# Kernel optimization log

Hardware: AMD Instinct MI355X
Metric: run time of the kernel (lower is better)

## Reference

```python
import jax, jax.numpy as jnp
import numpy as np
from functools import partial

NPOINT, NSAMPLE = 1024, 32
EPS = 1e-5

def setup_inputs() -> dict:
    key = jax.random.key(0)
    ks = jax.random.split(key, 16)
    B, N, C = 16, 4096, 64
    d = {
        "xyz": jax.random.normal(ks[0], (B, N, 3), jnp.float32),
        "points": jax.random.normal(ks[1], (B, N, C), jnp.float32),
    }
    chans = [67, 64, 64, 128]
    for i in range(3):
        cin, cout = chans[i], chans[i + 1]
        d[f"w{i+1}"] = jax.random.normal(ks[2 + i], (cout, cin), jnp.float32) * (1.0 / np.sqrt(cin))
        d[f"b{i+1}"] = jnp.zeros((cout,), jnp.float32)
        d[f"g{i+1}"] = jnp.ones((cout,), jnp.float32)
        d[f"be{i+1}"] = jnp.zeros((cout,), jnp.float32)
    return d

def farthest_point_sample(xyz, npoint):
    # xyz: (B, N, 3); deterministic start index 0 (torch code uses randint)
    B, N, _ = xyz.shape
    bidx = jnp.arange(B)

    def step(carry, _):
        distance, farthest = carry
        centroid = xyz[bidx, farthest]                       # (B, 3)
        dist = jnp.sum((xyz - centroid[:, None, :]) ** 2, -1)  # (B, N)
        distance = jnp.minimum(distance, dist)
        return (distance, jnp.argmax(distance, axis=1)), farthest

    init = (jnp.full((B, N), 1e10, xyz.dtype), jnp.zeros((B,), jnp.int32))
    _, centroids = jax.lax.scan(step, init, None, length=npoint)  # (npoint, B)
    return centroids.T                                            # (B, npoint)

def knn_group(nsample, xyz, new_xyz, points):
    # xyz: (B,N,3), new_xyz: (B,S,3), points: (B,N,C)
    # squared distances (same topk ordering as cdist)
    d2 = (jnp.sum(new_xyz ** 2, -1)[:, :, None]
          + jnp.sum(xyz ** 2, -1)[:, None, :]
          - 2.0 * jnp.einsum("bsd,bnd->bsn", new_xyz, xyz))     # (B,S,N)
    _, idx = jax.lax.top_k(-d2, nsample)                          # (B,S,K)

    gather = jax.vmap(lambda feats, i: feats[i])                  # per-batch fancy index
    grouped_xyz = gather(xyz, idx) - new_xyz[:, :, None, :]       # (B,S,K,3)
    grouped_pts = jnp.concatenate([grouped_xyz, gather(points, idx)], -1)  # (B,S,K,3+C)
    return grouped_xyz, grouped_pts

def mlp_layer(x, w, b, g, be):
    # 1x1 conv + BatchNorm (batch stats, training mode) + ReLU
    y = jnp.einsum("bskc,oc->bsko", x, w) + b
    mu = jnp.mean(y, axis=(0, 1, 2))
    var = jnp.var(y, axis=(0, 1, 2))
    y = (y - mu) * jax.lax.rsqrt(var + EPS) * g + be
    return jax.nn.relu(y)

def reference(xyz, points, w1, b1, g1, be1, w2, b2, g2, be2, w3, b3, g3, be3):
    centroids = farthest_point_sample(xyz, NPOINT)                    # (B,S)
    new_xyz = jnp.take_along_axis(xyz, centroids[:, :, None], axis=1)  # (B,S,3)
    _, x = knn_group(NSAMPLE, xyz, new_xyz, points)                   # (B,S,K,3+C)
    x = mlp_layer(x, w1, b1, g1, be1)
    x = mlp_layer(x, w2, b2, g2, be2)
    x = mlp_layer(x, w3, b3, g3, be3)
    new_points = jnp.max(x, axis=2)                                   # (B,S,mlp[-1])
    return new_xyz, new_points
```

## Files before the change

kernel.cpp:

```cpp
#include <hip/hip_runtime.h>

typedef unsigned int   uint;
typedef unsigned short ushort;
typedef unsigned long long u64;
typedef float f32x4 __attribute__((ext_vector_type(4)));

__device__ __forceinline__ void dot16x2(const float* __restrict__ wr,
                                        const f32x4* xa, const f32x4* xb,
                                        float& accA, float& accB){
#pragma unroll
  for (int k=0;k<4;k++){
    f32x4 w=*(const f32x4*)(wr+4*k);
    accA=fmaf(xa[k][0],w[0],accA); accA=fmaf(xa[k][1],w[1],accA);
    accA=fmaf(xa[k][2],w[2],accA); accA=fmaf(xa[k][3],w[3],accA);
    accB=fmaf(xb[k][0],w[0],accB); accB=fmaf(xb[k][1],w[1],accB);
    accB=fmaf(xb[k][2],w[2],accB); accB=fmaf(xb[k][3],w[3],accB);
  }
}

__global__ __launch_bounds__(256) void k_fps(const float* __restrict__ xyz,
                                             int* __restrict__ cent,
                                             float* __restrict__ oxyz){
  __shared__ __align__(16) float sp[4096][4];
  __shared__ u64 rk[2][4];
  __shared__ int sel[1024];
  const int b = blockIdx.x, tid = threadIdx.x, lane=tid&63, wave=tid>>6;
  const float* xb = xyz + (long)b*4096*3;
  float px[16], py[16], pz[16], pd[16];
#pragma unroll
  for (int j=0;j<16;j++){
    int n = tid + 256*j;
    float x=xb[n*3], y=xb[n*3+1], z=xb[n*3+2];
    sp[n][0]=x; sp[n][1]=y; sp[n][2]=z; sp[n][3]=0.0f;
    px[j]=x; py[j]=y; pz[j]=z; pd[j]=1e10f;
  }
  if (tid==0) sel[0]=0;
  __syncthreads();
  int f = 0;
  for (int t=1;t<1024;t++){
    f32x4 c = *(const f32x4*)sp[f];
    float bv=-1.0f; int bi=0;
#pragma unroll
    for (int j=0;j<16;j++){
      int n = tid + 256*j;
      float dx=px[j]-c[0], dy=py[j]-c[1], dz=pz[j]-c[2];
      float d=__fadd_rn(__fadd_rn(__fmul_rn(dx,dx),__fmul_rn(dy,dy)),__fmul_rn(dz,dz));
      float mn=fminf(pd[j],d); pd[j]=mn;
      if (j==0){ bv=mn; bi=n; }
      else if (mn>bv){ bv=mn; bi=n; }
    }
    u64 key = ((u64)__float_as_uint(bv)<<32) | (uint)(~bi);
#pragma unroll
    for (int off=32;off;off>>=1){
      u64 ok=__shfl_xor(key,off);
      key = ok>key ? ok : key;
    }
    int par=t&1;
    if (lane==0) rk[par][wave]=key;
    __syncthreads();
    {
      u64 k0=rk[par][0], k1=rk[par][1], k2=rk[par][2], k3=rk[par][3];
      u64 ka = k0>k1?k0:k1;
      u64 kb = k2>k3?k2:k3;
      u64 kk = ka>kb?ka:kb;
      f = (int)(~(uint)kk) & 4095;
    }
    if (tid==0) sel[t]=f;
  }
  __syncthreads();
#pragma unroll
  for (int j=0;j<4;j++){
    int s = tid + 256*j;
    int n = sel[s];
    cent[b*1024+s]=n;
    f32x4 cf=*(const f32x4*)sp[n];
    oxyz[(b*1024+s)*3+0]=cf[0];
    oxyz[(b*1024+s)*3+1]=cf[1];
    oxyz[(b*1024+s)*3+2]=cf[2];
  }
}

__global__ __launch_bounds__(256) void k_knn(const float* __restrict__ xyz,
                                             const int* __restrict__ cent,
                                             ushort* __restrict__ kidx){
  __shared__ float sx[4096], sy[4096], sz[4096];
  const int bx=blockIdx.x, b=bx>>5, chunk=bx&31;
  const int tid=threadIdx.x, lane=tid&63, wave=tid>>6;
  const float* xb = xyz + (long)b*4096*3;
#pragma unroll
  for (int j=0;j<16;j++){
    int n = tid + 256*j;
    sx[n]=xb[n*3]; sy[n]=xb[n*3+1]; sz[n]=xb[n*3+2];
  }
  __syncthreads();
  const u64 SENT=~0ull;
  for (int qi=0; qi<8; qi++){
    int s = chunk*32 + wave*8 + qi;
    int qn = cent[b*1024 + s] & 4095;
    double qx=(double)sx[qn], qy=(double)sy[qn], qz=(double)sz[qn];
    u64 k1=SENT, k2=SENT;
#pragma unroll 8
    for (int j=0;j<64;j++){
      int n = lane + 64*j;
      double dx=(double)sx[n]-qx, dy=(double)sy[n]-qy, dz=(double)sz[n]-qz;
      double d2 = dx*dx + dy*dy + dz*dz;
      u64 kd = (((u64)__double_as_longlong(d2)) & ~4095ull) | (uint)n;
      if (kd<k1){ k2=k1; k1=kd; }
      else if (kd<k2){ k2=kd; }
    }
    u64 removed=0ull;
    ushort* outp = kidx + (b*1024 + s)*32;
    for (int r=0;r<32;r++){
      u64 wk=k1;
#pragma unroll
      for (int off=32;off;off>>=1){
        u64 ok=__shfl_xor(wk,off);
        wk = ok<wk ? ok : wk;
      }
      if (lane==0) outp[r]=(ushort)(wk & 4095u);
      if (wk==k1){
        removed |= 1ull << (((uint)(k1&4095u))>>6);
        if (k2!=SENT){ k1=k2; k2=SENT; }
        else {
          k1=SENT; k2=SENT;
#pragma unroll 8
          for (int j=0;j<64;j++){
            if ((removed>>j)&1ull) continue;
            int n = lane + 64*j;
            double dx=(double)sx[n]-qx, dy=(double)sy[n]-qy, dz=(double)sz[n]-qz;
            double d2 = dx*dx + dy*dy + dz*dz;
            u64 kd = (((u64)__double_as_longlong(d2)) & ~4095ull) | (uint)n;
            if (kd<k1){ k2=k1; k1=kd; }
            else if (kd<k2){ k2=kd; }
          }
        }
      }
    }
  }
}


__global__ __launch_bounds__(256) void k_mlp1b(const float* __restrict__ xyz,
                                               const float* __restrict__ pts,
                                               const float* __restrict__ w1,
                                               const float* __restrict__ b1,
                                               const int* __restrict__ cent,
                                               const ushort* __restrict__ kidx,
                                               float* __restrict__ part,
                                               float* __restrict__ y){
  __shared__ __align__(16) float L[9760];
  float* W1  = L;
  float* XIN = L+4384;
  float* WRED= L+8736;
  const int tid=threadIdx.x, bi=blockIdx.x;
  const int row=tid>>3, oc=tid&7, wave=tid>>6;
  const int b=bi>>6, s0=(bi&63)*16;
  const long bN=(long)b*4096;

  for (int i=tid;i<64*68;i+=256){
    int r=i/68, c=i-r*68;
    float v = (c<64)? w1[r*67+3+c] : (c<67? w1[r*67+(c-64)] : 0.0f);
    W1[r*68+((r>>3)<<2)+c]=v;
  }
  float breg1[8];
#pragma unroll
  for (int i=0;i<8;i++) breg1[i]=b1[oc*8+i];
  float ps[8], pq[8];
#pragma unroll
  for (int s=0;s<8;s++){ ps[s]=0.f; pq[s]=0.f; }
  __syncthreads();

  for (int t=0; t<8; t++){
    int sgA = b*1024 + s0 + t*2, sgB = sgA+1;
    {
      int nA = kidx[sgA*32+row] & 4095;
      int nB = kidx[sgB*32+row] & 4095;
      const float* prA = pts + (bN+nA)*64;
      const float* prB = pts + (bN+nB)*64;
      *(f32x4*)(XIN + row*68 + oc*8)          = *(const f32x4*)(prA + oc*8);
      *(f32x4*)(XIN + row*68 + oc*8 + 4)      = *(const f32x4*)(prA + oc*8 + 4);
      *(f32x4*)(XIN + (row+32)*68 + oc*8)     = *(const f32x4*)(prB + oc*8);
      *(f32x4*)(XIN + (row+32)*68 + oc*8 + 4) = *(const f32x4*)(prB + oc*8 + 4);
      if (oc==0){
        int qA = cent[sgA] & 4095, qB = cent[sgB] & 4095;
        const float* xpA = xyz + (bN+nA)*3; const float* qpA = xyz + (bN+qA)*3;
        const float* xpB = xyz + (bN+nB)*3; const float* qpB = xyz + (bN+qB)*3;
        XIN[row*68+64]=xpA[0]-qpA[0]; XIN[row*68+65]=xpA[1]-qpA[1];
        XIN[row*68+66]=xpA[2]-qpA[2]; XIN[row*68+67]=0.0f;
        XIN[(row+32)*68+64]=xpB[0]-qpB[0]; XIN[(row+32)*68+65]=xpB[1]-qpB[1];
        XIN[(row+32)*68+66]=xpB[2]-qpB[2]; XIN[(row+32)*68+67]=0.0f;
      }
    }
    const float* xrowA = XIN + row*68;
    const float* xrowB = XIN + (row+32)*68;
    float acc[2][8];
#pragma unroll
    for (int i=0;i<8;i++){ acc[0][i]=breg1[i]; acc[1][i]=breg1[i]; }
#pragma unroll
    for (int co=0;co<4;co++){
      f32x4 xa[4], xbv[4];
#pragma unroll
      for (int k=0;k<4;k++){ xa[k]=*(const f32x4*)(xrowA+co*16+4*k); xbv[k]=*(const f32x4*)(xrowB+co*16+4*k); }
#pragma unroll
      for (int i=0;i<8;i++)
        dot16x2(W1+(oc*8+i)*68+(oc<<2)+co*16, xa, xbv, acc[0][i], acc[1][i]);
    }
    {
      f32x4 xtA=*(const f32x4*)(xrowA+64), xtB=*(const f32x4*)(xrowB+64);
#pragma unroll
      for (int i=0;i<8;i++){
        const float* wr=W1+(oc*8+i)*68+(oc<<2)+64;
        f32x4 w=*(const f32x4*)wr;
        acc[0][i]=fmaf(xtA[0],w[0],acc[0][i]); acc[0][i]=fmaf(xtA[1],w[1],acc[0][i]);
        acc[0][i]=fmaf(xtA[2],w[2],acc[0][i]); acc[0][i]=fmaf(xtA[3],w[3],acc[0][i]);
        acc[1][i]=fmaf(xtB[0],w[0],acc[1][i]); acc[1][i]=fmaf(xtB[1],w[1],acc[1][i]);
        acc[1][i]=fmaf(xtB[2],w[2],acc[1][i]); acc[1][i]=fmaf(xtB[3],w[3],acc[1][i]);
      }
    }
    {
      long baseA = ((long)sgA*32+row)*64 + oc*8;
      long baseB = ((long)sgB*32+row)*64 + oc*8;
      *(f32x4*)(y+baseA)   = (f32x4){acc[0][0],acc[0][1],acc[0][2],acc[0][3]};
      *(f32x4*)(y+baseA+4) = (f32x4){acc[0][4],acc[0][5],acc[0][6],acc[0][7]};
      *(f32x4*)(y+baseB)   = (f32x4){acc[1][0],acc[1][1],acc[1][2],acc[1][3]};
      *(f32x4*)(y+baseB+4) = (f32x4){acc[1][4],acc[1][5],acc[1][6],acc[1][7]};
    }
#pragma unroll
    for (int i=0;i<8;i++){
      ps[i]+=acc[0][i]+acc[1][i];
      pq[i]=fmaf(acc[0][i],acc[0][i],pq[i]); pq[i]=fmaf(acc[1][i],acc[1][i],pq[i]);
    }
  }
#pragma unroll
  for (int s=0;s<8;s++){
    ps[s]+=__shfl_xor(ps[s],8); ps[s]+=__shfl_xor(ps[s],16); ps[s]+=__shfl_xor(ps[s],32);
    pq[s]+=__shfl_xor(pq[s],8); pq[s]+=__shfl_xor(pq[s],16); pq[s]+=__shfl_xor(pq[s],32);
  }
  __syncthreads();
  if ((tid&63)<8){
    for (int s=0;s<8;s++){
      WRED[((wave*8+oc)*16+s)*2+0]=ps[s];
      WRED[((wave*8+oc)*16+s)*2+1]=pq[s];
    }
  }
  __syncthreads();
  if (tid<64){
    int o=tid, occ=o>>3, i=o&7;
    float s=0.f,q=0.f;
#pragma unroll
    for (int w=0;w<4;w++){ s+=WRED[((w*8+occ)*16+i)*2]; q+=WRED[((w*8+occ)*16+i)*2+1]; }
    part[(bi*64+o)*2]=s; part[(bi*64+o)*2+1]=q;
  }
}

__global__ __launch_bounds__(256) void k_mlp2b(const float* __restrict__ w2,
                                               const float* __restrict__ b2,
                                               const float* __restrict__ ab1,
                                               float* __restrict__ part,
                                               float* __restrict__ y){
  __shared__ __align__(16) float L[9504];
  float* W2  = L;
  float* XIN = L+4128;
  float* WRED= L+8480;
  const int tid=threadIdx.x, bi=blockIdx.x;
  const int row=tid>>3, oc=tid&7, wave=tid>>6;
  const int b=bi>>6, s0=(bi&63)*16;

  for (int i=tid;i<4096;i+=256){
    int r=i>>6, c=i&63;
    W2[r*64+((r>>3)<<2)+c]=w2[i];
  }
  float areg1[8],creg1[8],breg2[8];
#pragma unroll
  for (int i=0;i<8;i++){ int ch=oc*8+i; areg1[i]=ab1[ch*2]; creg1[i]=ab1[ch*2+1]; breg2[i]=b2[ch]; }
  float ps[8], pq[8];
#pragma unroll
  for (int s=0;s<8;s++){ ps[s]=0.f; pq[s]=0.f; }
  __syncthreads();

  for (int t=0; t<8; t++){
    int sgA = b*1024 + s0 + t*2, sgB = sgA+1;
    long baseA = ((long)sgA*32+row)*64 + oc*8;
    long baseB = ((long)sgB*32+row)*64 + oc*8;
    {
      f32x4 ya0=*(const f32x4*)(y+baseA), ya1=*(const f32x4*)(y+baseA+4);
      f32x4 yb0=*(const f32x4*)(y+baseB), yb1=*(const f32x4*)(y+baseB+4);
      f32x4 xo;
      xo[0]=fmaxf(fmaf(areg1[0],ya0[0],creg1[0]),0.0f);
      xo[1]=fmaxf(fmaf(areg1[1],ya0[1],creg1[1]),0.0f);
      xo[2]=fmaxf(fmaf(areg1[2],ya0[2],creg1[2]),0.0f);
      xo[3]=fmaxf(fmaf(areg1[3],ya0[3],creg1[3]),0.0f);
      *(f32x4*)(XIN+row*68+oc*8)=xo;
      xo[0]=fmaxf(fmaf(areg1[4],ya1[0],creg1[4]),0.0f);
      xo[1]=fmaxf(fmaf(areg1[5],ya1[1],creg1[5]),0.0f);
      xo[2]=fmaxf(fmaf(areg1[6],ya1[2],creg1[6]),0.0f);
      xo[3]=fmaxf(fmaf(areg1[7],ya1[3],creg1[7]),0.0f);
      *(f32x4*)(XIN+row*68+oc*8+4)=xo;
      xo[0]=fmaxf(fmaf(areg1[0],yb0[0],creg1[0]),0.0f);
      xo[1]=fmaxf(fmaf(areg1[1],yb0[1],creg1[1]),0.0f);
      xo[2]=fmaxf(fmaf(areg1[2],yb0[2],creg1[2]),0.0f);
      xo[3]=fmaxf(fmaf(areg1[3],yb0[3],creg1[3]),0.0f);
      *(f32x4*)(XIN+(row+32)*68+oc*8)=xo;
      xo[0]=fmaxf(fmaf(areg1[4],yb1[0],creg1[4]),0.0f);
      xo[1]=fmaxf(fmaf(areg1[5],yb1[1],creg1[5]),0.0f);
      xo[2]=fmaxf(fmaf(areg1[6],yb1[2],creg1[6]),0.0f);
      xo[3]=fmaxf(fmaf(areg1[7],yb1[3],creg1[7]),0.0f);
      *(f32x4*)(XIN+(row+32)*68+oc*8+4)=xo;
    }
    const float* x2A = XIN + row*68;
    const float* x2B = XIN + (row+32)*68;
    float acc2[2][8];
#pragma unroll
    for (int i=0;i<8;i++){ acc2[0][i]=breg2[i]; acc2[1][i]=breg2[i]; }
#pragma unroll
    for (int co=0;co<4;co++){
      f32x4 xa[4], xbv[4];
#pragma unroll
      for (int k=0;k<4;k++){ xa[k]=*(const f32x4*)(x2A+co*16+4*k); xbv[k]=*(const f32x4*)(x2B+co*16+4*k); }
#pragma unroll
      for (int i=0;i<8;i++)
        dot16x2(W2+(oc*8+i)*64+(oc<<2)+co*16, xa, xbv, acc2[0][i], acc2[1][i]);
    }
    *(f32x4*)(y+baseA)   = (f32x4){acc2[0][0],acc2[0][1],acc2[0][2],acc2[0][3]};
    *(f32x4*)(y+baseA+4) = (f32x4){acc2[0][4],acc2[0][5],acc2[0][6],acc2[0][7]};
    *(f32x4*)(y+baseB)   = (f32x4){acc2[1][0],acc2[1][1],acc2[1][2],acc2[1][3]};
    *(f32x4*)(y+baseB+4) = (f32x4){acc2[1][4],acc2[1][5],acc2[1][6],acc2[1][7]};
#pragma unroll
    for (int i=0;i<8;i++){
      ps[i]+=acc2[0][i]+acc2[1][i];
      pq[i]=fmaf(acc2[0][i],acc2[0][i],pq[i]); pq[i]=fmaf(acc2[1][i],acc2[1][i],pq[i]);
    }
  }
#pragma unroll
  for (int s=0;s<8;s++){
    ps[s]+=__shfl_xor(ps[s],8); ps[s]+=__shfl_xor(ps[s],16); ps[s]+=__shfl_xor(ps[s],32);
    pq[s]+=__shfl_xor(pq[s],8); pq[s]+=__shfl_xor(pq[s],16); pq[s]+=__shfl_xor(pq[s],32);
  }
  __syncthreads();
  if ((tid&63)<8){
    for (int s=0;s<8;s++){
      WRED[((wave*8+oc)*16+s)*2+0]=ps[s];
      WRED[((wave*8+oc)*16+s)*2+1]=pq[s];
    }
  }
  __syncthreads();
  if (tid<64){
    int o=tid, occ=o>>3, i=o&7;
    float s=0.f,q=0.f;
#pragma unroll
    for (int w=0;w<4;w++){ s+=WRED[((w*8+occ)*16+i)*2]; q+=WRED[((w*8+occ)*16+i)*2+1]; }
    part[(bi*64+o)*2]=s; part[(bi*64+o)*2+1]=q;
  }
}

__global__ __launch_bounds__(256) void k_mlp3b(const float* __restrict__ w3,
                                               const float* __restrict__ b3,
                                               const float* __restrict__ ab2,
                                               float* __restrict__ part,
                                               const float* __restrict__ y,
                                               float* __restrict__ mx){
  __shared__ __align__(16) float L[13696];
  float* W3F = L;
  float* XIN = L+8320;
  float* WRED= L+12672;
  const int tid=threadIdx.x, bi=blockIdx.x;
  const int row=tid>>3, oc=tid&7, wave=tid>>6;
  const int b=bi>>6, s0=(bi&63)*16;

  for (int i=tid;i<8192;i+=256){
    int og=i>>11, rem=i&2047, r=rem>>6, c=rem&63;
    W3F[og*2080 + r*64+((r>>2)<<2)+c]=w3[i];
  }
  float areg2[8],creg2[8];
#pragma unroll
  for (int i=0;i<8;i++){ int ch=oc*8+i; areg2[i]=ab2[ch*2]; creg2[i]=ab2[ch*2+1]; }
  float breg3[16];
#pragma unroll
  for (int og=0;og<4;og++)
#pragma unroll
    for (int i=0;i<4;i++) breg3[og*4+i]=b3[og*32+oc*4+i];
  float ps[16], pq[16];
#pragma unroll
  for (int s=0;s<16;s++){ ps[s]=0.f; pq[s]=0.f; }
  __syncthreads();

  for (int t=0; t<8; t++){
    int sgA = b*1024 + s0 + t*2, sgB = sgA+1;
    long baseA = ((long)sgA*32+row)*64 + oc*8;
    long baseB = ((long)sgB*32+row)*64 + oc*8;
    {
      f32x4 ya0=*(const f32x4*)(y+baseA), ya1=*(const f32x4*)(y+baseA+4);
      f32x4 yb0=*(const f32x4*)(y+baseB), yb1=*(const f32x4*)(y+baseB+4);
      f32x4 xo;
      xo[0]=fmaxf(fmaf(areg2[0],ya0[0],creg2[0]),0.0f);
      xo[1]=fmaxf(fmaf(areg2[1],ya0[1],creg2[1]),0.0f);
      xo[2]=fmaxf(fmaf(areg2[2],ya0[2],creg2[2]),0.0f);
      xo[3]=fmaxf(fmaf(areg2[3],ya0[3],creg2[3]),0.0f);
      *(f32x4*)(XIN+row*68+oc*8)=xo;
      xo[0]=fmaxf(fmaf(areg2[4],ya1[0],creg2[4]),0.0f);
      xo[1]=fmaxf(fmaf(areg2[5],ya1[1],creg2[5]),0.0f);
      xo[2]=fmaxf(fmaf(areg2[6],ya1[2],creg2[6]),0.0f);
      xo[3]=fmaxf(fmaf(areg2[7],ya1[3],creg2[7]),0.0f);
      *(f32x4*)(XIN+row*68+oc*8+4)=xo;
      xo[0]=fmaxf(fmaf(areg2[0],yb0[0],creg2[0]),0.0f);
      xo[1]=fmaxf(fmaf(areg2[1],yb0[1],creg2[1]),0.0f);
      xo[2]=fmaxf(fmaf(areg2[2],yb0[2],creg2[2]),0.0f);
      xo[3]=fmaxf(fmaf(areg2[3],yb0[3],creg2[3]),0.0f);
      *(f32x4*)(XIN+(row+32)*68+oc*8)=xo;
      xo[0]=fmaxf(fmaf(areg2[4],yb1[0],creg2[4]),0.0f);
      xo[1]=fmaxf(fmaf(areg2[5],yb1[1],creg2[5]),0.0f);
      xo[2]=fmaxf(fmaf(areg2[6],yb1[2],creg2[6]),0.0f);
      xo[3]=fmaxf(fmaf(areg2[7],yb1[3],creg2[7]),0.0f);
      *(f32x4*)(XIN+(row+32)*68+oc*8+4)=xo;
    }
    const float* x2A = XIN + row*68;
    const float* x2B = XIN + (row+32)*68;
    float acc3[4][2][4];
#pragma unroll
    for (int og=0;og<4;og++)
#pragma unroll
      for (int i=0;i<4;i++){ acc3[og][0][i]=breg3[og*4+i]; acc3[og][1][i]=breg3[og*4+i]; }
#pragma unroll
    for (int co=0;co<4;co++){
      f32x4 xa[4], xbv[4];
#pragma unroll
      for (int k=0;k<4;k++){ xa[k]=*(const f32x4*)(x2A+co*16+4*k); xbv[k]=*(const f32x4*)(x2B+co*16+4*k); }
#pragma unroll
      for (int og=0;og<4;og++)
#pragma unroll
        for (int i=0;i<4;i++)
          dot16x2(W3F+og*2080+(oc*4+i)*64+(oc<<2)+co*16, xa, xbv, acc3[og][0][i], acc3[og][1][i]);
    }
    float vm[2][16];
#pragma unroll
    for (int og=0;og<4;og++)
#pragma unroll
      for (int i=0;i<4;i++){
        int s=og*4+i;
        ps[s]+=acc3[og][0][i]+acc3[og][1][i];
        pq[s]=fmaf(acc3[og][0][i],acc3[og][0][i],pq[s]); pq[s]=fmaf(acc3[og][1][i],acc3[og][1][i],pq[s]);
        vm[0][s]=acc3[og][0][i]; vm[1][s]=acc3[og][1][i];
      }
    {
#pragma unroll
      for (int q=0;q<2;q++)
#pragma unroll
        for (int s=0;s<16;s++){
          vm[q][s]=fmaxf(vm[q][s],__shfl_xor(vm[q][s],8));
          vm[q][s]=fmaxf(vm[q][s],__shfl_xor(vm[q][s],16));
          vm[q][s]=fmaxf(vm[q][s],__shfl_xor(vm[q][s],32));
        }
      __syncthreads();
      if ((tid&63)<8){
#pragma unroll
        for (int q=0;q<2;q++)
#pragma unroll
          for (int s=0;s<16;s++) WRED[(q*32 + wave*8+oc)*16 + s]=vm[q][s];
      }
      __syncthreads();
      {
        int q=tid>>7, o=tid&127;
        int og=o>>5, occ=(o&31)>>2, s=og*4+(o&3);
        float v=WRED[(q*32 + 0*8+occ)*16+s];
        v=fmaxf(v,WRED[(q*32 + 1*8+occ)*16+s]);
        v=fmaxf(v,WRED[(q*32 + 2*8+occ)*16+s]);
        v=fmaxf(v,WRED[(q*32 + 3*8+occ)*16+s]);
        mx[(long)(q? sgB : sgA)*128+o]=v;
      }
    }
  }
  {
#pragma unroll
    for (int s=0;s<16;s++){
      ps[s]+=__shfl_xor(ps[s],8); ps[s]+=__shfl_xor(ps[s],16); ps[s]+=__shfl_xor(ps[s],32);
      pq[s]+=__shfl_xor(pq[s],8); pq[s]+=__shfl_xor(pq[s],16); pq[s]+=__shfl_xor(pq[s],32);
    }
    __syncthreads();
    if ((tid&63)<8){
      for (int s=0;s<16;s++){
        WRED[((wave*8+oc)*16+s)*2+0]=ps[s];
        WRED[((wave*8+oc)*16+s)*2+1]=pq[s];
      }
    }
    __syncthreads();
    if (tid<128){
      int o=tid, og=o>>5, occ=(o&31)>>2, i=o&3, s2=og*4+i;
      float s=0.f,q=0.f;
#pragma unroll
      for (int w=0;w<4;w++){ s+=WRED[((w*8+occ)*16+s2)*2]; q+=WRED[((w*8+occ)*16+s2)*2+1]; }
      part[(bi*128+o)*2]=s; part[(bi*128+o)*2+1]=q;
    }
  }
}

__global__ void k_red(const float* __restrict__ part,
                      const float* __restrict__ gam,
                      const float* __restrict__ bet,
                      float* __restrict__ ab, int nch, int nblk){
  __shared__ float red[4][128][2];
  const int tid=threadIdx.x, ch=tid%nch, seg=tid/nch;
  float s=0.f,q=0.f;
  for (int i=seg;i<nblk;i+=4){ s+=part[(i*nch+ch)*2]; q+=part[(i*nch+ch)*2+1]; }
  red[seg][ch][0]=s; red[seg][ch][1]=q;
  __syncthreads();
  if (seg==0){
    s=red[0][ch][0]+red[1][ch][0]+red[2][ch][0]+red[3][ch][0];
    q=red[0][ch][1]+red[1][ch][1]+red[2][ch][1]+red[3][ch][1];
    float mu=s*(1.0f/524288.0f);
    float var=q*(1.0f/524288.0f)-mu*mu;
    var=fmaxf(var,0.0f);
    float a=gam[ch]/sqrtf(var+1e-5f);
    float c=bet[ch]-mu*a;
    ab[ch*2]=a; ab[ch*2+1]=c;
  }
}

__global__ __launch_bounds__(256) void k_out(const float* __restrict__ mx,
                                             const float* __restrict__ ab3,
                                             float* __restrict__ onp){
  int i = (blockIdx.x*256 + threadIdx.x)*4;
  int ch = i & 127;
  f32x4 v = *(const f32x4*)(mx+i);
  f32x4 r;
  r[0]=fmaxf(fmaf(ab3[(ch+0)*2], v[0], ab3[(ch+0)*2+1]), 0.0f);
  r[1]=fmaxf(fmaf(ab3[(ch+1)*2], v[1], ab3[(ch+1)*2+1]), 0.0f);
  r[2]=fmaxf(fmaf(ab3[(ch+2)*2], v[2], ab3[(ch+2)*2+1]), 0.0f);
  r[3]=fmaxf(fmaf(ab3[(ch+3)*2], v[3], ab3[(ch+3)*2+1]), 0.0f);
  *(f32x4*)(onp+i)=r;
}

extern "C" void kernel_launch(void* const* d_in, const int* in_sizes, int n_in,
                              void* d_out, int out_size, void* d_ws, size_t ws_size,
                              hipStream_t stream){
  const float* xyz=(const float*)d_in[0];
  const float* pts=(const float*)d_in[1];
  const float* w1 =(const float*)d_in[2];
  const float* b1 =(const float*)d_in[3];
  const float* g1 =(const float*)d_in[4];
  const float* be1=(const float*)d_in[5];
  const float* w2 =(const float*)d_in[6];
  const float* b2 =(const float*)d_in[7];
  const float* g2 =(const float*)d_in[8];
  const float* be2=(const float*)d_in[9];
  const float* w3 =(const float*)d_in[10];
  const float* b3 =(const float*)d_in[11];
  const float* g3 =(const float*)d_in[12];
  const float* be3=(const float*)d_in[13];
  char* ws=(char*)d_ws;
  int*    cent=(int*)(ws);
  ushort* kidx=(ushort*)(ws+  65536);
  float*  p   =(float*)(ws+ 1114112);
  float*  ab1 =(float*)(ws+ 2162688);
  float*  ab2 =(float*)(ws+ 2163200);
  float*  ab3 =(float*)(ws+ 2163712);
  float*  mx  =(float*)(ws+ 2164736);
  float*  y   =(float*)(ws+16777216);
  float* oxyz=(float*)d_out;
  float* onp =oxyz + 16*1024*3;

  const bool bigws = ws_size >= 150994944ull;

  k_fps<<<16, 256, 0, stream>>>(xyz, cent, oxyz);
  k_knn<<<512, 256, 0, stream>>>(xyz, cent, kidx);
  if (bigws){
    k_mlp1b<<<1024, 256, 0, stream>>>(xyz, pts, w1, b1, cent, kidx, p, y);
    k_red<<<1, 256, 0, stream>>>(p, g1, be1, ab1, 64, 1024);
    k_mlp2b<<<1024, 256, 0, stream>>>(w2, b2, ab1, p, y);
    k_red<<<1, 256, 0, stream>>>(p, g2, be2, ab2, 64, 1024);
    k_mlp3b<<<1024, 256, 0, stream>>>(w3, b3, ab2, p, y, mx);
    k_red<<<1, 512, 0, stream>>>(p, g3, be3, ab3, 128, 1024);
  } else {
    k_mlp1b<<<1024, 256, 0, stream>>>(xyz, pts, w1, b1, cent, kidx, p, y);
    k_red<<<1, 256, 0, stream>>>(p, g1, be1, ab1, 64, 1024);
    k_mlp2b<<<1024, 256, 0, stream>>>(w2, b2, ab1, p, y);
    k_red<<<1, 256, 0, stream>>>(p, g2, be2, ab2, 64, 1024);
    k_mlp3b<<<1024, 256, 0, stream>>>(w3, b3, ab2, p, y, mx);
    k_red<<<1, 512, 0, stream>>>(p, g3, be3, ab3, 128, 1024);
  }
  k_out<<<2048, 256, 0, stream>>>(mx, ab3, onp);
}
```

Baseline: 2.031 ms.

## Fuse FPS and KNN into one persistent kernel with per-batch ready flags

Merges the farthest-point-sampling and KNN kernels into a single launch: the first 16 blocks run FPS per batch and publish a release flag, while the remaining blocks loop over KNN work units and spin-wait on the flag for their batch. This aims to remove the kernel boundary and let KNN work overlap with FPS tails. It adds a memset for the flags and relies on FPS blocks being resident before waiting blocks, which risks deadlock or waiting blocks occupying CUs during FPS.

After: 2.548 ms. 1.25x slower.

```diff
diff --git a/kernel.cpp b/kernel.cpp
--- a/kernel.cpp
+++ b/kernel.cpp
@@ -18,127 +18,140 @@
   }
 }
 
-__global__ __launch_bounds__(256) void k_fps(const float* __restrict__ xyz,
-                                             int* __restrict__ cent,
-                                             float* __restrict__ oxyz){
-  __shared__ __align__(16) float sp[4096][4];
-  __shared__ u64 rk[2][4];
-  __shared__ int sel[1024];
-  const int b = blockIdx.x, tid = threadIdx.x, lane=tid&63, wave=tid>>6;
-  const float* xb = xyz + (long)b*4096*3;
-  float px[16], py[16], pz[16], pd[16];
-#pragma unroll
-  for (int j=0;j<16;j++){
-    int n = tid + 256*j;
-    float x=xb[n*3], y=xb[n*3+1], z=xb[n*3+2];
-    sp[n][0]=x; sp[n][1]=y; sp[n][2]=z; sp[n][3]=0.0f;
-    px[j]=x; py[j]=y; pz[j]=z; pd[j]=1e10f;
-  }
-  if (tid==0) sel[0]=0;
-  __syncthreads();
-  int f = 0;
-  for (int t=1;t<1024;t++){
-    f32x4 c = *(const f32x4*)sp[f];
-    float bv=-1.0f; int bi=0;
+__global__ __launch_bounds__(256,2) void k_fk(const float* __restrict__ xyz,
+                                              int* __restrict__ cent,
+                                              float* __restrict__ oxyz,
+                                              ushort* __restrict__ kidx,
+                                              int* __restrict__ flags){
+  __shared__ __align__(16) char LU[69760];
+  const int bid=blockIdx.x, tid=threadIdx.x, lane=tid&63, wave=tid>>6;
+
+  if (bid < 16){
+    float (*sp)[4] = (float(*)[4])LU;
+    u64* rk  = (u64*)(LU + 65536);
+    int* sel = (int*)(LU + 65600);
+    const int b = bid;
+    const float* xb = xyz + (long)b*4096*3;
+    float px[16], py[16], pz[16], pd[16];
 #pragma unroll
     for (int j=0;j<16;j++){
       int n = tid + 256*j;
-      float dx=px[j]-c[0], dy=py[j]-c[1], dz=pz[j]-c[2];
-      float d=__fadd_rn(__fadd_rn(__fmul_rn(dx,dx),__fmul_rn(dy,dy)),__fmul_rn(dz,dz));
-      float mn=fminf(pd[j],d); pd[j]=mn;
-      if (j==0){ bv=mn; bi=n; }
-      else if (mn>bv){ bv=mn; bi=n; }
-    }
-    u64 key = ((u64)__float_as_uint(bv)<<32) | (uint)(~bi);
-#pragma unroll
-    for (int off=32;off;off>>=1){
-      u64 ok=__shfl_xor(key,off);
-      key = ok>key ? ok : key;
-    }
-    int par=t&1;
-    if (lane==0) rk[par][wave]=key;
+      float x=xb[n*3], y=xb[n*3+1], z=xb[n*3+2];
+      sp[n][0]=x; sp[n][1]=y; sp[n][2]=z; sp[n][3]=0.0f;
+      px[j]=x; py[j]=y; pz[j]=z; pd[j]=1e10f;
+    }
+    if (tid==0) sel[0]=0;
     __syncthreads();
-    {
-      u64 k0=rk[par][0], k1=rk[par][1], k2=rk[par][2], k3=rk[par][3];
-      u64 ka = k0>k1?k0:k1;
-      u64 kb = k2>k3?k2:k3;
-      u64 kk = ka>kb?ka:kb;
-      f = (int)(~(uint)kk) & 4095;
-    }
-    if (tid==0) sel[t]=f;
-  }
-  __syncthreads();
-#pragma unroll
-  for (int j=0;j<4;j++){
-    int s = tid + 256*j;
-    int n = sel[s];
-    cent[b*1024+s]=n;
-    f32x4 cf=*(const f32x4*)sp[n];
-    oxyz[(b*1024+s)*3+0]=cf[0];
-    oxyz[(b*1024+s)*3+1]=cf[1];
-    oxyz[(b*1024+s)*3+2]=cf[2];
-  }
-}
-
-__global__ __launch_bounds__(256) void k_knn(const float* __restrict__ xyz,
-                                             const int* __restrict__ cent,
-                                             ushort* __restrict__ kidx){
-  __shared__ float sx[4096], sy[4096], sz[4096];
-  const int bx=blockIdx.x, b=bx>>5, chunk=bx&31;
-  const int tid=threadIdx.x, lane=tid&63, wave=tid>>6;
-  const float* xb = xyz + (long)b*4096*3;
-#pragma unroll
-  for (int j=0;j<16;j++){
-    int n = tid + 256*j;
-    sx[n]=xb[n*3]; sy[n]=xb[n*3+1]; sz[n]=xb[n*3+2];
-  }
-  __syncthreads();
-  const u64 SENT=~0ull;
-  for (int qi=0; qi<8; qi++){
-    int s = chunk*32 + wave*8 + qi;
-    int qn = cent[b*1024 + s] & 4095;
-    double qx=(double)sx[qn], qy=(double)sy[qn], qz=(double)sz[qn];
-    u64 k1=SENT, k2=SENT;
+    int f = 0;
+    for (int t=1;t<1024;t++){
+      f32x4 c = *(const f32x4*)sp[f];
+      float bv=-1.0f; int bi=0;
+#pragma unroll
+      for (int j=0;j<16;j++){
+        int n = tid + 256*j;
+        float dx=px[j]-c[0], dy=py[j]-c[1], dz=pz[j]-c[2];
+        float d=__fadd_rn(__fadd_rn(__fmul_rn(dx,dx),__fmul_rn(dy,dy)),__fmul_rn(dz,dz));
+        float mn=fminf(pd[j],d); pd[j]=mn;
+        if (j==0){ bv=mn; bi=n; }
+        else if (mn>bv){ bv=mn; bi=n; }
+      }
+      u64 key = ((u64)__float_as_uint(bv)<<32) | (uint)(~bi);
+#pragma unroll
+      for (int off=32;off;off>>=1){
+        u64 ok=__shfl_xor(key,off);
+        key = ok>key ? ok : key;
+      }
+      int par=t&1;
+      if (lane==0) rk[par*4+wave]=key;
+      __syncthreads();
+      {
+        u64 k0=rk[par*4+0], k1=rk[par*4+1], k2=rk[par*4+2], k3=rk[par*4+3];
+        u64 ka = k0>k1?k0:k1;
+        u64 kb = k2>k3?k2:k3;
+        u64 kk = ka>kb?ka:kb;
+        f = (int)(~(uint)kk) & 4095;
+      }
+      if (tid==0) sel[t]=f;
+    }
+    __syncthreads();
+#pragma unroll
+    for (int j=0;j<4;j++){
+      int s = tid + 256*j;
+      int n = sel[s];
+      cent[b*1024+s]=n;
+      f32x4 cf=*(const f32x4*)sp[n];
+      oxyz[(b*1024+s)*3+0]=cf[0];
+      oxyz[(b*1024+s)*3+1]=cf[1];
+      oxyz[(b*1024+s)*3+2]=cf[2];
+    }
+    __threadfence();
+    __syncthreads();
+    if (tid==0)
+      __hip_atomic_store(&flags[b], 1, __ATOMIC_RELEASE, __HIP_MEMORY_SCOPE_AGENT);
+  } else {
+    float* sx=(float*)LU; float* sy=sx+4096; float* sz=sy+4096;
+    for (int u = bid-16; u < 512; u += 496){
+      const int b = u>>5, chunk = u&31;
+      if (tid==0){
+        while (__hip_atomic_load(&flags[b], __ATOMIC_ACQUIRE, __HIP_MEMORY_SCOPE_AGENT)==0)
+          __builtin_amdgcn_s_sleep(64);
+      }
+      __syncthreads();
+      const float* xb = xyz + (long)b*4096*3;
+#pragma unroll
+      for (int j=0;j<16;j++){
+        int n = tid + 256*j;
+        sx[n]=xb[n*3]; sy[n]=xb[n*3+1]; sz[n]=xb[n*3+2];
+      }
+      __syncthreads();
+      const u64 SENT=~0ull;
+      for (int qi=0; qi<8; qi++){
+        int s = chunk*32 + wave*8 + qi;
+        int qn = cent[b*1024 + s] & 4095;
+        double qx=(double)sx[qn], qy=(double)sy[qn], qz=(double)sz[qn];
+        u64 k1=SENT, k2=SENT;
 #pragma unroll 8
-    for (int j=0;j<64;j++){
-      int n = lane + 64*j;
-      double dx=(double)sx[n]-qx, dy=(double)sy[n]-qy, dz=(double)sz[n]-qz;
-      double d2 = dx*dx + dy*dy + dz*dz;
-      u64 kd = (((u64)__double_as_longlong(d2)) & ~4095ull) | (uint)n;
-      if (kd<k1){ k2=k1; k1=kd; }
-      else if (kd<k2){ k2=kd; }
-    }
-    u64 removed=0ull;
-    ushort* outp = kidx + (b*1024 + s)*32;
-    for (int r=0;r<32;r++){
-      u64 wk=k1;
-#pragma unroll
-      for (int off=32;off;off>>=1){
-        u64 ok=__shfl_xor(wk,off);
-        wk = ok<wk ? ok : wk;
-      }
-      if (lane==0) outp[r]=(ushort)(wk & 4095u);
-      if (wk==k1){
-        removed |= 1ull << (((uint)(k1&4095u))>>6);
-        if (k2!=SENT){ k1=k2; k2=SENT; }
-        else {
-          k1=SENT; k2=SENT;
+        for (int j=0;j<64;j++){
+          int n = lane + 64*j;
+          double dx=(double)sx[n]-qx, dy=(double)sy[n]-qy, dz=(double)sz[n]-qz;
+          double d2 = dx*dx + dy*dy + dz*dz;
+          u64 kd = (((u64)__double_as_longlong(d2)) & ~4095ull) | (uint)n;
+          if (kd<k1){ k2=k1; k1=kd; }
+          else if (kd<k2){ k2=kd; }
+        }
+        u64 removed=0ull;
+        ushort* outp = kidx + (b*1024 + s)*32;
+        for (int r=0;r<32;r++){
+          u64 wk=k1;
+#pragma unroll
+          for (int off=32;off;off>>=1){
+            u64 ok=__shfl_xor(wk,off);
+            wk = ok<wk ? ok : wk;
+          }
+          if (lane==0) outp[r]=(ushort)(wk & 4095u);
+          if (wk==k1){
+            removed |= 1ull << (((uint)(k1&4095u))>>6);
+            if (k2!=SENT){ k1=k2; k2=SENT; }
+            else {
+              k1=SENT; k2=SENT;
 #pragma unroll 8
-          for (int j=0;j<64;j++){
-            if ((removed>>j)&1ull) continue;
-            int n = lane + 64*j;
-            double dx=(double)sx[n]-qx, dy=(double)sy[n]-qy, dz=(double)sz[n]-qz;
-            double d2 = dx*dx + dy*dy + dz*dz;
-            u64 kd = (((u64)__double_as_longlong(d2)) & ~4095ull) | (uint)n;
-            if (kd<k1){ k2=k1; k1=kd; }
-            else if (kd<k2){ k2=kd; }
+              for (int j=0;j<64;j++){
+                if ((removed>>j)&1ull) continue;
+                int n = lane + 64*j;
+                double dx=(double)sx[n]-qx, dy=(double)sy[n]-qy, dz=(double)sz[n]-qz;
+                double d2 = dx*dx + dy*dy + dz*dz;
+                u64 kd = (((u64)__double_as_longlong(d2)) & ~4095ull) | (uint)n;
+                if (kd<k1){ k2=k1; k1=kd; }
+                else if (kd<k2){ k2=kd; }
+              }
+            }
           }
         }
       }
-    }
-  }
-}
-
+      __syncthreads();
+    }
+  }
+}
 
 __global__ __launch_bounds__(256) void k_mlp1b(const float* __restrict__ xyz,
                                                const float* __restrict__ pts,
@@ -554,28 +567,18 @@
   float*  ab2 =(float*)(ws+ 2163200);
   float*  ab3 =(float*)(ws+ 2163712);
   float*  mx  =(float*)(ws+ 2164736);
+  int*    flags=(int*)(ws+15728640);
   float*  y   =(float*)(ws+16777216);
   float* oxyz=(float*)d_out;
   float* onp =oxyz + 16*1024*3;
 
-  const bool bigws = ws_size >= 150994944ull;
-
-  k_fps<<<16, 256, 0, stream>>>(xyz, cent, oxyz);
-  k_knn<<<512, 256, 0, stream>>>(xyz, cent, kidx);
-  if (bigws){
-    k_mlp1b<<<1024, 256, 0, stream>>>(xyz, pts, w1, b1, cent, kidx, p, y);
-    k_red<<<1, 256, 0, stream>>>(p, g1, be1, ab1, 64, 1024);
-    k_mlp2b<<<1024, 256, 0, stream>>>(w2, b2, ab1, p, y);
-    k_red<<<1, 256, 0, stream>>>(p, g2, be2, ab2, 64, 1024);
-    k_mlp3b<<<1024, 256, 0, stream>>>(w3, b3, ab2, p, y, mx);
-    k_red<<<1, 512, 0, stream>>>(p, g3, be3, ab3, 128, 1024);
-  } else {
-    k_mlp1b<<<1024, 256, 0, stream>>>(xyz, pts, w1, b1, cent, kidx, p, y);
-    k_red<<<1, 256, 0, stream>>>(p, g1, be1, ab1, 64, 1024);
-    k_mlp2b<<<1024, 256, 0, stream>>>(w2, b2, ab1, p, y);
-    k_red<<<1, 256, 0, stream>>>(p, g2, be2, ab2, 64, 1024);
-    k_mlp3b<<<1024, 256, 0, stream>>>(w3, b3, ab2, p, y, mx);
-    k_red<<<1, 512, 0, stream>>>(p, g3, be3, ab3, 128, 1024);
-  }
+  hipMemsetAsync(flags, 0, 64, stream);
+  k_fk<<<512, 256, 0, stream>>>(xyz, cent, oxyz, kidx, flags);
+  k_mlp1b<<<1024, 256, 0, stream>>>(xyz, pts, w1, b1, cent, kidx, p, y);
+  k_red<<<1, 256, 0, stream>>>(p, g1, be1, ab1, 64, 1024);
+  k_mlp2b<<<1024, 256, 0, stream>>>(w2, b2, ab1, p, y);
+  k_red<<<1, 256, 0, stream>>>(p, g2, be2, ab2, 64, 1024);
+  k_mlp3b<<<1024, 256, 0, stream>>>(w3, b3, ab2, p, y, mx);
+  k_red<<<1, 512, 0, stream>>>(p, g3, be3, ab3, 128, 1024);
   k_out<<<2048, 256, 0, stream>>>(mx, ab3, onp);
 }
```
